# Performance work log

Hardware: AMD Instinct MI355X
Metric: run time of the kernel (lower is better)

## Reference

```python
import jax, jax.numpy as jnp
import numpy as np

N_USERS = 100000
N_ITEMS = 50000
N_NODES = N_USERS + N_ITEMS
EMB_DIM = 64
NNZ = 4800000
BATCH = 4096
N_LAYERS = 3


def setup_inputs() -> dict:
    key = jax.random.key(0)
    k1, k2, k3, k4, k5, k6, k7, k8 = jax.random.split(key, 8)
    edge_row = jax.random.randint(k1, (NNZ,), 0, N_NODES, dtype=jnp.int32)
    edge_col = jax.random.randint(k2, (NNZ,), 0, N_NODES, dtype=jnp.int32)
    # normalized adjacency values are positive, ~1/sqrt(deg_i*deg_j)
    edge_val = jax.random.uniform(k3, (NNZ,), dtype=jnp.float32) * (2.0 / 32.0)
    user_emb = jax.random.normal(k4, (N_USERS, EMB_DIM), dtype=jnp.float32) * 0.1
    item_emb = jax.random.normal(k5, (N_ITEMS, EMB_DIM), dtype=jnp.float32) * 0.1
    users = jax.random.randint(k6, (BATCH,), 0, N_USERS, dtype=jnp.int64)
    pos_items = jax.random.randint(k7, (BATCH,), 0, N_ITEMS, dtype=jnp.int64)
    neg_items = jax.random.randint(k8, (BATCH,), 0, N_ITEMS, dtype=jnp.int64)
    return {
        "edge_row": edge_row,
        "edge_col": edge_col,
        "edge_val": edge_val,
        "user_emb": user_emb,
        "item_emb": item_emb,
        "users": users,
        "pos_items": pos_items,
        "neg_items": neg_items,
    }


def reference(edge_row, edge_col, edge_val, user_emb, item_emb, users, pos_items, neg_items):
    n_users = user_emb.shape[0]
    n_nodes = n_users + item_emb.shape[0]
    # ego embeddings: [N, D]
    ego = jnp.concatenate([user_emb, item_emb], axis=0)
    acc = ego  # running sum over layers (layer 0 included)
    for _ in range(N_LAYERS):
        # SpMM: out[r] = sum_{e: row[e]==r} val[e] * ego[col[e]]
        msg = edge_val[:, None] * ego[edge_col]          # [nnz, D]
        ego = jax.ops.segment_sum(msg, edge_row, num_segments=n_nodes)
        acc = acc + ego
    all_emb = acc / (N_LAYERS + 1)                       # layer average
    u_all = all_emb[:n_users]
    i_all = all_emb[n_users:]
    u_g = u_all[users]
    pos_i_g = i_all[pos_items]
    neg_i_g = i_all[neg_items]
    return (u_g, pos_i_g, neg_i_g)
```

## Files before the change

### kernel.cpp

```cpp
#include <hip/hip_runtime.h>

#define N_USERS 100000
#define N_ITEMS 50000
#define N_NODES 150000
#define EMB 64
#define NNZ_TOT 4800000
#define BATCH_SZ 4096

#define BROWS 64
#define NB 2344
#define CHUNKS 512
#define CHUNKE 9375
#define SBUF 3072
#define BIN_LDS (2 * NB * 4 + CHUNKE * 8)
#define VOFF (112u << 23)

typedef unsigned short u16;

static __device__ __forceinline__ u16 f2bf(float f) {
    unsigned u = __float_as_uint(f);
    unsigned r = u + 0x7FFFu + ((u >> 16) & 1u);
    return (u16)(r >> 16);
}
static __device__ __forceinline__ float bf2f(u16 h) {
    return __uint_as_float(((unsigned)h) << 16);
}

__global__ void k_init(const float* __restrict__ ue, const float* __restrict__ ie,
                       u16* __restrict__ ego) {
    size_t i = (size_t)blockIdx.x * blockDim.x + threadIdx.x;
    const size_t n4 = (size_t)N_NODES * EMB / 4;
    if (i >= n4) return;
    const size_t u4 = (size_t)N_USERS * EMB / 4;
    float4 v = (i < u4) ? ((const float4*)ue)[i] : ((const float4*)ie)[i - u4];
    ushort4 o;
    o.x = f2bf(v.x); o.y = f2bf(v.y); o.z = f2bf(v.z); o.w = f2bf(v.w);
    ((ushort4*)ego)[i] = o;
}

__global__ void k_zero(int* __restrict__ p, int n) {
    int i = blockIdx.x * blockDim.x + threadIdx.x;
    if (i < n) p[i] = 0;
}

__global__ __launch_bounds__(1024) void k_bin(const int* __restrict__ erow,
                                              const int* __restrict__ ecol,
                                              const float* __restrict__ eval_,
                                              int2* __restrict__ pairsA,
                                              int* __restrict__ off_t,
                                              int* __restrict__ bucketCnt) {
    extern __shared__ int smem[];
    int*  hist = smem;
    int*  fill = smem + NB;
    int2* buf  = (int2*)(smem + 2 * NB);
    const int c = blockIdx.x;
    const int cbase = c * CHUNKE;
    const int tid = threadIdx.x;

    for (int i = tid; i < NB; i += 1024) hist[i] = 0;
    __syncthreads();

    for (int i = tid; i < CHUNKE; i += 1024)
        atomicAdd(&hist[erow[cbase + i] >> 6], 1);
    __syncthreads();

    if (tid < 64) {
        int carry = 0;
        for (int blk = 0; blk < (NB + 63) / 64; ++blk) {
            int idx = blk * 64 + tid;
            int v = (idx < NB) ? hist[idx] : 0;
            int s = v;
            #pragma unroll
            for (int o = 1; o < 64; o <<= 1) {
                int t = __shfl_up(s, o);
                if (tid >= o) s += t;
            }
            if (idx < NB) fill[idx] = s - v + carry;
            carry += __shfl(s, 63);
        }
    }
    __syncthreads();

    for (int i = tid; i < NB; i += 1024) {
        off_t[i * CHUNKS + c] = cbase + fill[i];
        atomicAdd(&bucketCnt[i], hist[i]);
    }
    if (tid == 0) off_t[NB * CHUNKS + c] = cbase + CHUNKE;
    __syncthreads();

    for (int i = tid; i < CHUNKE; i += 1024) {
        int e = cbase + i;
        int r = erow[e];
        int bb = r >> 6;
        int p = atomicAdd(&fill[bb], 1);
        int2 pr;
        pr.x = ((r & 63) << 18) | ecol[e];
        pr.y = __float_as_int(eval_[e]);
        buf[p] = pr;
    }
    __syncthreads();

    for (int i = tid; i < CHUNKE; i += 1024)
        pairsA[cbase + i] = buf[i];
}

__global__ __launch_bounds__(1024) void k_bscan(const int* __restrict__ cnt,
                                                int* __restrict__ bbase,
                                                int* __restrict__ rowptr) {
    __shared__ int lds[1024];
    const int tid = threadIdx.x;
    int vals[3];
    int local = 0;
    #pragma unroll
    for (int j = 0; j < 3; ++j) {
        int idx = tid * 3 + j;
        int v = (idx < NB) ? cnt[idx] : 0;
        vals[j] = local;
        local += v;
    }
    lds[tid] = local;
    __syncthreads();
    for (int off = 1; off < 1024; off <<= 1) {
        int t = (tid >= off) ? lds[tid - off] : 0;
        __syncthreads();
        lds[tid] += t;
        __syncthreads();
    }
    int excl = lds[tid] - local;
    #pragma unroll
    for (int j = 0; j < 3; ++j) {
        int idx = tid * 3 + j;
        if (idx <= NB) {
            int b = excl + vals[j];
            bbase[idx] = b;
            if (idx == NB) rowptr[N_NODES] = b;
        }
    }
}

__global__ __launch_bounds__(256) void k_sort(const int* __restrict__ off_t,
                                              const int2* __restrict__ pairsA,
                                              const int* __restrict__ bbase,
                                              unsigned* __restrict__ pairsB,
                                              int* __restrict__ rowptr) {
    __shared__ int hist[BROWS];
    __shared__ int fillx[BROWS];
    __shared__ int segstart[512];
    __shared__ int segbase[512];
    __shared__ int2 buf[SBUF];
    __shared__ int wsum[4];
    const int b = blockIdx.x;
    const int tid = threadIdx.x, lane = tid & 63, w = tid >> 6;

    const int s0 = off_t[b * CHUNKS + tid];
    const int e0 = off_t[(b + 1) * CHUNKS + tid];
    const int s1 = off_t[b * CHUNKS + tid + 256];
    const int e1 = off_t[(b + 1) * CHUNKS + tid + 256];
    const int l0 = e0 - s0;
    const int len = l0 + (e1 - s1);

    if (tid < BROWS) hist[tid] = 0;

    int sc = len;
    #pragma unroll
    for (int o = 1; o < 64; o <<= 1) {
        int t = __shfl_up(sc, o);
        if (lane >= o) sc += t;
    }
    if (lane == 63) wsum[w] = sc;
    __syncthreads();
    int wbase = 0;
    for (int i = 0; i < w; ++i) wbase += wsum[i];
    int tbase = wbase + sc - len;

    segbase[2 * tid]     = tbase;
    segbase[2 * tid + 1] = tbase + l0;
    segstart[2 * tid]     = s0;
    segstart[2 * tid + 1] = s1;
    __syncthreads();

    const int base = bbase[b];
    int total = bbase[b + 1] - base;
    if (total > SBUF) total = SBUF;

#define FINDSEG(j, idx)                                                        \
    {                                                                          \
        int lo = 0, hi = 511;                                                  \
        while (lo < hi) {                                                      \
            int mid = (lo + hi + 1) >> 1;                                      \
            if (segbase[mid] <= (j)) lo = mid; else hi = mid - 1;              \
        }                                                                      \
        (idx) = segstart[lo] + ((j) - segbase[lo]);                            \
    }

    int j = tid;
    for (; j + 768 < total; j += 1024) {
        int i0, i1, i2, i3;
        FINDSEG(j,       i0)
        FINDSEG(j + 256, i1)
        FINDSEG(j + 512, i2)
        FINDSEG(j + 768, i3)
        int2 p0 = pairsA[i0];
        int2 p1 = pairsA[i1];
        int2 p2 = pairsA[i2];
        int2 p3 = pairsA[i3];
        buf[j]       = p0; atomicAdd(&hist[p0.x >> 18], 1);
        buf[j + 256] = p1; atomicAdd(&hist[p1.x >> 18], 1);
        buf[j + 512] = p2; atomicAdd(&hist[p2.x >> 18], 1);
        buf[j + 768] = p3; atomicAdd(&hist[p3.x >> 18], 1);
    }
    for (; j < total; j += 256) {
        int idx;
        FINDSEG(j, idx)
        int2 p = pairsA[idx];
        buf[j] = p;
        atomicAdd(&hist[p.x >> 18], 1);
    }
#undef FINDSEG
    __syncthreads();

    if (tid < 64) {
        int v = hist[tid];
        int s2 = v;
        #pragma unroll
        for (int o = 1; o < 64; o <<= 1) {
            int t = __shfl_up(s2, o);
            if (tid >= o) s2 += t;
        }
        int excl = s2 - v;
        fillx[tid] = excl;
        int node = b * BROWS + tid;
        if (node < N_NODES) rowptr[node] = base + excl;
    }
    __syncthreads();

    for (int i = tid; i < total; i += 256) {
        int2 p = buf[i];
        int pos = atomicAdd(&fillx[p.x >> 18], 1);
        unsigned bits = (unsigned)p.y;
        unsigned q;
        if (bits >= VOFF) {
            q = (bits + 4096u - VOFF) >> 13;
            if (q > 16383u) q = 16383u;
        } else q = 0;
        pairsB[base + pos] = (q << 18) | ((unsigned)p.x & 0x3FFFFu);
    }
}

__global__ __launch_bounds__(256) void k_spmv(const int* __restrict__ rowptr,
                                              const unsigned* __restrict__ pairs,
                                              const u16* __restrict__ cur,
                                              u16* __restrict__ nxt) {
    size_t gid = (size_t)blockIdx.x * blockDim.x + threadIdx.x;
    int pr   = (int)(gid >> 6);
    int lane = (int)(gid & 63);
    int rowA = pr * 2;
    if (rowA >= N_NODES) return;
    const int      sl  = lane & 31;
    const bool     hi  = lane >= 32;
    const unsigned sl4 = (unsigned)sl << 2;
    const char* tab = (const char*)cur;
    const unsigned* pl = pairs + (hi ? 1 : 0);

    int sA = rowptr[rowA];
    int mA = rowptr[rowA + 1];
    int eBnd = rowptr[rowA + 2];

    float a0 = 0.f, a1 = 0.f, b0 = 0.f, b1 = 0.f;
    float c0 = 0.f, c1 = 0.f, d0 = 0.f, d1 = 0.f;

#define PROC(wv, x0, x1)                                                       \
    {                                                                          \
        unsigned col = (wv) & 0x3FFFFu;                                        \
        float vv = __uint_as_float((((wv) >> 18) << 13) + VOFF);               \
        unsigned u = *(const unsigned*)(tab + (size_t)((col << 7) | sl4));     \
        x0 += vv * __uint_as_float(u << 16);                                   \
        x1 += vv * __uint_as_float(u & 0xFFFF0000u);                           \
    }
#define PROC1(wv, x0, x1)                                                      \
    {                                                                          \
        unsigned col = (wv) & 0x3FFFFu;                                        \
        float vv = __uint_as_float((((wv) >> 18) << 13) + VOFF);               \
        unsigned u = *(const unsigned*)(tab + (size_t)((col << 7) | sl4));     \
        float vm = hi ? 0.f : vv;                                              \
        x0 += vm * __uint_as_float(u << 16);                                   \
        x1 += vm * __uint_as_float(u & 0xFFFF0000u);                           \
    }

    int eA = sA, eB = mA;
    while (eA + 7 < mA && eB + 7 < eBnd) {
        unsigned A0 = pl[eA],     A1 = pl[eA + 2], A2 = pl[eA + 4], A3 = pl[eA + 6];
        unsigned B0 = pl[eB],     B1 = pl[eB + 2], B2 = pl[eB + 4], B3 = pl[eB + 6];
        PROC(A0, a0, a1) PROC(B0, c0, c1)
        PROC(A1, b0, b1) PROC(B1, d0, d1)
        PROC(A2, a0, a1) PROC(B2, c0, c1)
        PROC(A3, b0, b1) PROC(B3, d0, d1)
        eA += 8; eB += 8;
    }
    for (; eA + 7 < mA; eA += 8) {
        unsigned q0 = pl[eA], q1 = pl[eA + 2], q2 = pl[eA + 4], q3 = pl[eA + 6];
        PROC(q0, a0, a1) PROC(q1, b0, b1) PROC(q2, a0, a1) PROC(q3, b0, b1)
    }
    for (; eA + 1 < mA; eA += 2) {
        unsigned q = pl[eA];
        PROC(q, a0, a1)
    }
    if (eA < mA) { unsigned q = pairs[eA]; PROC1(q, a0, a1) }
    for (; eB + 7 < eBnd; eB += 8) {
        unsigned q0 = pl[eB], q1 = pl[eB + 2], q2 = pl[eB + 4], q3 = pl[eB + 6];
        PROC(q0, c0, c1) PROC(q1, d0, d1) PROC(q2, c0, c1) PROC(q3, d0, d1)
    }
    for (; eB + 1 < eBnd; eB += 2) {
        unsigned q = pl[eB];
        PROC(q, c0, c1)
    }
    if (eB < eBnd) { unsigned q = pairs[eB]; PROC1(q, c0, c1) }
#undef PROC
#undef PROC1

    float s0 = a0 + b0, s1 = a1 + b1;
    float t0 = c0 + d0, t1 = c1 + d1;
    s0 += __shfl_xor(s0, 32);
    s1 += __shfl_xor(s1, 32);
    t0 += __shfl_xor(t0, 32);
    t1 += __shfl_xor(t1, 32);
    if (!hi) {
        unsigned oA = (unsigned)f2bf(s0) | ((unsigned)f2bf(s1) << 16);
        unsigned oB = (unsigned)f2bf(t0) | ((unsigned)f2bf(t1) << 16);
        ((unsigned*)nxt)[(size_t)rowA * 32 + sl] = oA;
        ((unsigned*)nxt)[(size_t)(rowA + 1) * 32 + sl] = oB;
    }
}

__global__ void k_out1(const float* __restrict__ ue, const float* __restrict__ ie,
                       const u16* __restrict__ ego1,
                       const int* __restrict__ users, const int* __restrict__ pos,
                       const int* __restrict__ neg, float* __restrict__ out) {
    size_t t = (size_t)blockIdx.x * blockDim.x + threadIdx.x;
    size_t r = t >> 4;
    int sub = (int)(t & 15);
    if (r >= (size_t)(3 * BATCH_SZ)) return;
    int which = (int)(r / BATCH_SZ);
    int bi    = (int)(r % BATCH_SZ);
    int node;
    if (which == 0)      node = users[bi];
    else if (which == 1) node = N_USERS + pos[bi];
    else                 node = N_USERS + neg[bi];
    const float* src = (node < N_USERS) ? (ue + (size_t)node * EMB)
                                        : (ie + (size_t)(node - N_USERS) * EMB);
    float4 v = ((const float4*)src)[sub];
    ushort4 h = ((const ushort4*)(ego1 + (size_t)node * EMB))[sub];
    v.x += bf2f(h.x); v.y += bf2f(h.y); v.z += bf2f(h.z); v.w += bf2f(h.w);
    ((float4*)(out + r * EMB))[sub] = v;
}

#define RFL(x) __builtin_amdgcn_readfirstlane(x)
__global__ __launch_bounds__(256) void k_last(const int* __restrict__ rowptr,
                                              const unsigned* __restrict__ pairs,
                                              const u16* __restrict__ cur,
                                              const int* __restrict__ users,
                                              const int* __restrict__ pos,
                                              const int* __restrict__ neg,
                                              float* __restrict__ out) {
    size_t gid = (size_t)blockIdx.x * blockDim.x + threadIdx.x;
    int r    = (int)(gid >> 6);
    int lane = (int)(gid & 63);
    if (r >= 3 * BATCH_SZ) return;
    int which = r / BATCH_SZ;
    int bi    = r % BATCH_SZ;
    int node;
    if (which == 0)      node = users[bi];
    else if (which == 1) node = N_USERS + pos[bi];
    else                 node = N_USERS + neg[bi];
    int start = rowptr[node];
    int end   = rowptr[node + 1];
    float a0 = 0.f, a1 = 0.f, a2 = 0.f, a3 = 0.f;
    int e = start;
    for (; e + 3 < end; e += 4) {
        unsigned w0 = RFL(pairs[e]);
        unsigned w1 = RFL(pairs[e + 1]);
        unsigned w2 = RFL(pairs[e + 2]);
        unsigned w3 = RFL(pairs[e + 3]);
        float v0 = __uint_as_float(((w0 >> 18) << 13) + VOFF);
        float v1 = __uint_as_float(((w1 >> 18) << 13) + VOFF);
        float v2 = __uint_as_float(((w2 >> 18) << 13) + VOFF);
        float v3 = __uint_as_float(((w3 >> 18) << 13) + VOFF);
        a0 += v0 * bf2f(cur[(size_t)(w0 & 0x3FFFFu) * EMB + lane]);
        a1 += v1 * bf2f(cur[(size_t)(w1 & 0x3FFFFu) * EMB + lane]);
        a2 += v2 * bf2f(cur[(size_t)(w2 & 0x3FFFFu) * EMB + lane]);
        a3 += v3 * bf2f(cur[(size_t)(w3 & 0x3FFFFu) * EMB + lane]);
    }
    for (; e < end; ++e) {
        unsigned w = RFL(pairs[e]);
        float v = __uint_as_float(((w >> 18) << 13) + VOFF);
        a0 += v * bf2f(cur[(size_t)(w & 0x3FFFFu) * EMB + lane]);
    }
    float l2 = bf2f(cur[(size_t)node * EMB + lane]);
    float sum = (a0 + a1) + (a2 + a3) + l2;
    size_t oi = (size_t)r * EMB + lane;
    out[oi] = (out[oi] + sum) * 0.25f;
}

extern "C" void kernel_launch(void* const* d_in, const int* in_sizes, int n_in,
                              void* d_out, int out_size, void* d_ws, size_t ws_size,
                              hipStream_t stream) {
    const int*   erow  = (const int*)  d_in[0];
    const int*   ecol  = (const int*)  d_in[1];
    const float* eval_ = (const float*)d_in[2];
    const float* ue    = (const float*)d_in[3];
    const float* ie    = (const float*)d_in[4];
    const int*   users = (const int*)  d_in[5];
    const int*   pos   = (const int*)  d_in[6];
    const int*   neg   = (const int*)  d_in[7];
    float* out = (float*)d_out;

    char* ws = (char*)d_ws;
    const size_t tblB  = (size_t)150016 * EMB * sizeof(u16);
    const size_t pairB = (size_t)NNZ_TOT * sizeof(int2);
    u16*  ego0   = (u16*)(ws);
    u16*  ego1   = (u16*)(ws + tblB);
    int2* pairsA = (int2*)(ws);
    unsigned* pairsB = (unsigned*)(ws + 2 * tblB);
    int*  off_t  = (int*) (ws + 2 * tblB + pairB);
    int*  rowptr = off_t + (size_t)(NB + 1) * CHUNKS;
    int*  bucketCnt = rowptr + ((N_NODES + 1 + 63) & ~63);
    int*  bbase     = bucketCnt + NB;

    const int blk = 256;

    hipFuncSetAttribute(reinterpret_cast<const void*>(k_bin),
                        hipFuncAttributeMaxDynamicSharedMemorySize, BIN_LDS);

    k_zero<<<(NB + blk - 1) / blk, blk, 0, stream>>>(bucketCnt, NB);
    k_bin<<<CHUNKS, 1024, BIN_LDS, stream>>>(erow, ecol, eval_, pairsA, off_t, bucketCnt);
    k_bscan<<<1, 1024, 0, stream>>>(bucketCnt, bbase, rowptr);
    k_sort<<<NB, blk, 0, stream>>>(off_t, pairsA, bbase, pairsB, rowptr);

    const size_t n4 = (size_t)N_NODES * EMB / 4;
    k_init<<<(int)((n4 + blk - 1) / blk), blk, 0, stream>>>(ue, ie, ego0);

    const size_t spmv_threads = (size_t)(N_NODES / 2) * 64;
    const int grid_spmv = (int)((spmv_threads + blk - 1) / blk);
    const int grid_g = (int)(((size_t)3 * BATCH_SZ * 16 + blk - 1) / blk);

    k_spmv<<<grid_spmv, blk, 0, stream>>>(rowptr, pairsB, ego0, ego1);
    k_out1<<<grid_g, blk, 0, stream>>>(ue, ie, ego1, users, pos, neg, out);
    k_spmv<<<grid_spmv, blk, 0, stream>>>(rowptr, pairsB, ego1, ego0);

    const size_t lth = (size_t)3 * BATCH_SZ * 64;
    k_last<<<(int)((lth + blk - 1) / blk), blk, 0, stream>>>(rowptr, pairsB, ego0,
                                                             users, pos, neg, out);
}
```

Measured before the change: 315.7 us.

## Use smaller bin chunks, cache rows in LDS, split final gather across half-waves

The binning kernel now uses more, smaller chunks (960 of 5000 edges) and keeps each chunk's row indices in LDS so they are not read from global memory a second time. The sort kernel is generalized to merge up to 4 segments per thread for the new chunk count. The last-layer gather kernel now has each half-wave process alternate edges, with each lane loading two bf16 values as one 32-bit word, and the halves are combined with a cross-lane shuffle. The intent is more parallelism in binning and fewer redundant loads, at the cost of a larger offset table and a longer binary search in the sort kernel.

```diff
diff --git a/kernel.cpp b/kernel.cpp
--- a/kernel.cpp
+++ b/kernel.cpp
@@ -9,10 +9,10 @@
 
 #define BROWS 64
 #define NB 2344
-#define CHUNKS 512
-#define CHUNKE 9375
+#define CHUNKS 960
+#define CHUNKE 5000
 #define SBUF 3072
-#define BIN_LDS (2 * NB * 4 + CHUNKE * 8)
+#define BIN_LDS (2 * NB * 4 + CHUNKE * 4 + CHUNKE * 8)
 #define VOFF (112u << 23)
 
 typedef unsigned short u16;
@@ -52,7 +52,8 @@
     extern __shared__ int smem[];
     int*  hist = smem;
     int*  fill = smem + NB;
-    int2* buf  = (int2*)(smem + 2 * NB);
+    int*  rbuf = smem + 2 * NB;
+    int2* buf  = (int2*)(smem + 2 * NB + CHUNKE);
     const int c = blockIdx.x;
     const int cbase = c * CHUNKE;
     const int tid = threadIdx.x;
@@ -60,8 +61,11 @@
     for (int i = tid; i < NB; i += 1024) hist[i] = 0;
     __syncthreads();
 
-    for (int i = tid; i < CHUNKE; i += 1024)
-        atomicAdd(&hist[erow[cbase + i] >> 6], 1);
+    for (int i = tid; i < CHUNKE; i += 1024) {
+        int r = erow[cbase + i];
+        rbuf[i] = r;
+        atomicAdd(&hist[r >> 6], 1);
+    }
     __syncthreads();
 
     if (tid < 64) {
@@ -90,7 +94,7 @@
 
     for (int i = tid; i < CHUNKE; i += 1024) {
         int e = cbase + i;
-        int r = erow[e];
+        int r = rbuf[i];
         int bb = r >> 6;
         int p = atomicAdd(&fill[bb], 1);
         int2 pr;
@@ -145,19 +149,25 @@
                                               int* __restrict__ rowptr) {
     __shared__ int hist[BROWS];
     __shared__ int fillx[BROWS];
-    __shared__ int segstart[512];
-    __shared__ int segbase[512];
+    __shared__ int segstart[CHUNKS];
+    __shared__ int segbase[CHUNKS];
     __shared__ int2 buf[SBUF];
     __shared__ int wsum[4];
     const int b = blockIdx.x;
     const int tid = threadIdx.x, lane = tid & 63, w = tid >> 6;
 
-    const int s0 = off_t[b * CHUNKS + tid];
-    const int e0 = off_t[(b + 1) * CHUNKS + tid];
-    const int s1 = off_t[b * CHUNKS + tid + 256];
-    const int e1 = off_t[(b + 1) * CHUNKS + tid + 256];
-    const int l0 = e0 - s0;
-    const int len = l0 + (e1 - s1);
+    int sst[4], slen[4];
+    int len = 0;
+    #pragma unroll
+    for (int j = 0; j < 4; ++j) {
+        int sidx = 4 * tid + j;
+        if (sidx < CHUNKS) {
+            int s = off_t[b * CHUNKS + sidx];
+            int e = off_t[(b + 1) * CHUNKS + sidx];
+            sst[j] = s; slen[j] = e - s;
+        } else { sst[j] = 0; slen[j] = 0; }
+        len += slen[j];
+    }
 
     if (tid < BROWS) hist[tid] = 0;
 
@@ -171,12 +181,17 @@
     __syncthreads();
     int wbase = 0;
     for (int i = 0; i < w; ++i) wbase += wsum[i];
-    int tbase = wbase + sc - len;
-
-    segbase[2 * tid]     = tbase;
-    segbase[2 * tid + 1] = tbase + l0;
-    segstart[2 * tid]     = s0;
-    segstart[2 * tid + 1] = s1;
+    int run = wbase + sc - len;
+
+    #pragma unroll
+    for (int j = 0; j < 4; ++j) {
+        int sidx = 4 * tid + j;
+        if (sidx < CHUNKS) {
+            segbase[sidx] = run;
+            segstart[sidx] = sst[j];
+            run += slen[j];
+        }
+    }
     __syncthreads();
 
     const int base = bbase[b];
@@ -185,7 +200,7 @@
 
 #define FINDSEG(j, idx)                                                        \
     {                                                                          \
-        int lo = 0, hi = 511;                                                  \
+        int lo = 0, hi = CHUNKS - 1;                                           \
         while (lo < hi) {                                                      \
             int mid = (lo + hi + 1) >> 1;                                      \
             if (segbase[mid] <= (j)) lo = mid; else hi = mid - 1;              \
@@ -354,7 +369,6 @@
     ((float4*)(out + r * EMB))[sub] = v;
 }
 
-#define RFL(x) __builtin_amdgcn_readfirstlane(x)
 __global__ __launch_bounds__(256) void k_last(const int* __restrict__ rowptr,
                                               const unsigned* __restrict__ pairs,
                                               const u16* __restrict__ cur,
@@ -372,33 +386,48 @@
     if (which == 0)      node = users[bi];
     else if (which == 1) node = N_USERS + pos[bi];
     else                 node = N_USERS + neg[bi];
+    const int sl = lane & 31;
+    const bool hi = lane >= 32;
+    const unsigned sl4 = (unsigned)sl << 2;
+    const char* tab = (const char*)cur;
     int start = rowptr[node];
-    int end   = rowptr[node + 1];
-    float a0 = 0.f, a1 = 0.f, a2 = 0.f, a3 = 0.f;
-    int e = start;
-    for (; e + 3 < end; e += 4) {
-        unsigned w0 = RFL(pairs[e]);
-        unsigned w1 = RFL(pairs[e + 1]);
-        unsigned w2 = RFL(pairs[e + 2]);
-        unsigned w3 = RFL(pairs[e + 3]);
-        float v0 = __uint_as_float(((w0 >> 18) << 13) + VOFF);
-        float v1 = __uint_as_float(((w1 >> 18) << 13) + VOFF);
-        float v2 = __uint_as_float(((w2 >> 18) << 13) + VOFF);
-        float v3 = __uint_as_float(((w3 >> 18) << 13) + VOFF);
-        a0 += v0 * bf2f(cur[(size_t)(w0 & 0x3FFFFu) * EMB + lane]);
-        a1 += v1 * bf2f(cur[(size_t)(w1 & 0x3FFFFu) * EMB + lane]);
-        a2 += v2 * bf2f(cur[(size_t)(w2 & 0x3FFFFu) * EMB + lane]);
-        a3 += v3 * bf2f(cur[(size_t)(w3 & 0x3FFFFu) * EMB + lane]);
-    }
-    for (; e < end; ++e) {
-        unsigned w = RFL(pairs[e]);
-        float v = __uint_as_float(((w >> 18) << 13) + VOFF);
-        a0 += v * bf2f(cur[(size_t)(w & 0x3FFFFu) * EMB + lane]);
-    }
-    float l2 = bf2f(cur[(size_t)node * EMB + lane]);
-    float sum = (a0 + a1) + (a2 + a3) + l2;
-    size_t oi = (size_t)r * EMB + lane;
-    out[oi] = (out[oi] + sum) * 0.25f;
+    int n = rowptr[node + 1] - start;
+    const unsigned* pl = pairs + start + (hi ? 1 : 0);
+    int nh = hi ? (n >> 1) : ((n + 1) >> 1);
+
+    float a0 = 0.f, a1 = 0.f, b0 = 0.f, b1 = 0.f;
+#define PROC(wv, x0, x1)                                                       \
+    {                                                                          \
+        unsigned col = (wv) & 0x3FFFFu;                                        \
+        float vv = __uint_as_float((((wv) >> 18) << 13) + VOFF);               \
+        unsigned u = *(const unsigned*)(tab + (size_t)((col << 7) | sl4));     \
+        x0 += vv * __uint_as_float(u << 16);                                   \
+        x1 += vv * __uint_as_float(u & 0xFFFF0000u);                           \
+    }
+    int i = 0;
+    for (; i + 3 < nh; i += 4) {
+        unsigned q0 = pl[2 * i], q1 = pl[2 * i + 2];
+        unsigned q2 = pl[2 * i + 4], q3 = pl[2 * i + 6];
+        PROC(q0, a0, a1) PROC(q1, b0, b1) PROC(q2, a0, a1) PROC(q3, b0, b1)
+    }
+    for (; i < nh; ++i) {
+        unsigned q = pl[2 * i];
+        PROC(q, a0, a1)
+    }
+#undef PROC
+    float s0 = a0 + b0, s1 = a1 + b1;
+    s0 += __shfl_xor(s0, 32);
+    s1 += __shfl_xor(s1, 32);
+    if (!hi) {
+        unsigned u = *(const unsigned*)(tab + (((size_t)node) << 7) + sl4);
+        s0 += __uint_as_float(u << 16);
+        s1 += __uint_as_float(u & 0xFFFF0000u);
+        float2* op = (float2*)(out + (size_t)r * EMB) + sl;
+        float2 o = *op;
+        o.x = (o.x + s0) * 0.25f;
+        o.y = (o.y + s1) * 0.25f;
+        *op = o;
+    }
 }
 
 extern "C" void kernel_launch(void* const* d_in, const int* in_sizes, int n_in,
```

After: 334.9 us. +6.1%, slower.
